# Kernel tuning notes

Hardware: AMD Instinct MI355X
Metric: run time of the kernel (lower is better)

Reference implementation:

```python
import jax, jax.numpy as jnp
import numpy as np

N = 100000      # nodes
E = 1600000     # edges (before self-loops)
IN = 128        # in_size
H = 4           # heads
C = 32          # out_size // heads
OUT = H * C     # 128
NEG_SLOPE = 0.2
LN_EPS = 1e-5
SM_EPS = 1e-16  # PyG softmax eps


def setup_inputs() -> dict:
    key = jax.random.key(0)
    ks = jax.random.split(key, 6)
    x = jax.random.normal(ks[0], (N, IN), dtype=jnp.float32)
    edge_index = jax.random.randint(ks[1], (2, E), 0, N, dtype=jnp.int64)
    W = jax.random.normal(ks[2], (IN, OUT), dtype=jnp.float32) * 0.05
    a_src = jax.random.normal(ks[3], (H, C), dtype=jnp.float32) * 0.05
    a_dst = jax.random.normal(ks[4], (H, C), dtype=jnp.float32) * 0.05
    bias = jnp.zeros((OUT,), dtype=jnp.float32)
    gamma = jnp.ones((OUT,), dtype=jnp.float32)
    beta = jnp.zeros((OUT,), dtype=jnp.float32)
    return {"x": x, "edge_index": edge_index, "W": W, "a_src": a_src,
            "a_dst": a_dst, "bias": bias, "gamma": gamma, "beta": beta}


def reference(x, edge_index, W, a_src, a_dst, bias, gamma, beta):
    n = x.shape[0]
    # add self loops (PyG GATConv default)
    loops = jnp.arange(n, dtype=edge_index.dtype)
    src = jnp.concatenate([edge_index[0], loops])  # [E+N]
    dst = jnp.concatenate([edge_index[1], loops])

    h = (x @ W).reshape(n, H, C)                   # [N,H,C]
    alpha_src = jnp.sum(h * a_src, axis=-1)        # [N,H]
    alpha_dst = jnp.sum(h * a_dst, axis=-1)        # [N,H]

    e = jax.nn.leaky_relu(alpha_src[src] + alpha_dst[dst], NEG_SLOPE)  # [E+N,H]
    # segment softmax over edges grouped by destination node
    emax = jax.ops.segment_max(e, dst, num_segments=n)
    emax = jnp.where(jnp.isfinite(emax), emax, 0.0)
    ee = jnp.exp(e - emax[dst])
    denom = jax.ops.segment_sum(ee, dst, num_segments=n)
    alpha = ee / (denom[dst] + SM_EPS)             # [E+N,H]

    msg = h[src] * alpha[:, :, None]               # [E+N,H,C]
    out = jax.ops.segment_sum(msg, dst, num_segments=n).reshape(n, OUT) + bias

    # LayerNorm(out_size)
    mu = jnp.mean(out, axis=-1, keepdims=True)
    var = jnp.var(out, axis=-1, keepdims=True)
    out = (out - mu) * jax.lax.rsqrt(var + LN_EPS) * gamma + beta
    return jax.nn.relu(out)
```

## Files before the change

kernel.cpp:

```cpp
#include <hip/hip_runtime.h>
#include <hip/hip_bf16.h>
#include <math.h>

#define IN_DIM 128
#define OUT_DIM 128
#define NHEAD 4
#define HC 32
#define NEG_SLOPE 0.2f
#define LN_EPS 1e-5f
#define SM_EPS 1e-16f

#define NB_SHIFT 9
#define BDST 512
#define NBUCK_MAX 256
#define BIN_ITER 28
#define BIN_CHUNK (BIN_ITER * 256)
#define SRC_BITS 17
#define SRC_MASK ((1u << SRC_BITS) - 1u)
#define BCAP_SHIFT 14
#define BCAP (1 << BCAP_SHIFT)

typedef __attribute__((ext_vector_type(8))) short bf16x8;
typedef __attribute__((ext_vector_type(4))) short short4v;
typedef __attribute__((ext_vector_type(4))) float f32x4;

__device__ __forceinline__ float leaky(float v) { return v > 0.f ? v : NEG_SLOPE * v; }

__device__ __forceinline__ short f2b(float f) {
    __hip_bfloat16 b = __float2bfloat16(f);
    return *reinterpret_cast<short*>(&b);
}
__device__ __forceinline__ float b2f(short s) {
    return __uint_as_float(((unsigned)(unsigned short)s) << 16);
}

__device__ __forceinline__ int swz(int row, int byteInRow) {
    return row * 256 + (byteInRow ^ ((row & 7) << 4));
}

__global__ void k_prepW(const float* __restrict__ W, __hip_bfloat16* __restrict__ WtB,
                        int* __restrict__ bcur)
{
    int t0 = blockIdx.x * 256 + threadIdx.x;
    int k = t0 >> 7, j = t0 & 127;
    WtB[j * IN_DIM + k] = __float2bfloat16(W[t0]);
    if (blockIdx.x == 0) bcur[threadIdx.x] = 0;
}

__global__ void __launch_bounds__(256)
k_gemm_bin(const float* __restrict__ x, const __hip_bfloat16* __restrict__ WtB,
           const float* __restrict__ a_src, const float* __restrict__ a_dst,
           __hip_bfloat16* __restrict__ hB, float* __restrict__ asrc_out,
           float* __restrict__ adst_out,
           const int* __restrict__ ei, int* __restrict__ bcur,
           unsigned* __restrict__ binned,
           int E, int N, int nblk_bin)
{
    __shared__ __align__(16) char lds[49152];
    const int t = threadIdx.x;

    if ((int)blockIdx.x < nblk_bin) {
        int* cnt = (int*)lds;
        int* gb  = (int*)(lds + 1024);
        int tot = E + N;
        int base = (int)blockIdx.x * BIN_CHUNK;

        cnt[t] = 0;
        __syncthreads();

        int rk[BIN_ITER], bk[BIN_ITER], dlo[BIN_ITER];
        #pragma unroll
        for (int k = 0; k < BIN_ITER; ++k) {
            int e = base + k * 256 + t;
            bk[k] = -1; rk[k] = 0; dlo[k] = 0;
            if (e < tot) {
                int d = (e < E) ? ei[E + e] : (e - E);
                bk[k] = d >> NB_SHIFT;
                dlo[k] = d & (BDST - 1);
                rk[k] = atomicAdd(&cnt[bk[k]], 1);
            }
        }
        __syncthreads();
        gb[t] = cnt[t] ? ((t << BCAP_SHIFT) + atomicAdd(&bcur[t], cnt[t])) : 0;
        __syncthreads();
        #pragma unroll
        for (int k = 0; k < BIN_ITER; ++k) {
            int e = base + k * 256 + t;
            if (e < tot) {
                int s = (e < E) ? ei[e] : (e - E);
                binned[gb[bk[k]] + rk[k]] = (unsigned)s | ((unsigned)dlo[k] << SRC_BITS);
            }
        }
    } else {
        const int node0 = ((int)blockIdx.x - nblk_bin) * 64;

        #pragma unroll
        for (int i = 0; i < 16; ++i) {
            int idx = (i * 256 + t) * 4;
            int col = idx >> 7, k = idx & 127;
            short4v w4 = *reinterpret_cast<const short4v*>((const short*)WtB + idx);
            *reinterpret_cast<short4v*>(lds + 16384 + swz(col, 2 * k)) = w4;
        }
        #pragma unroll
        for (int i = 0; i < 8; ++i) {
            int idx = (i * 256 + t) * 4;
            int row = idx >> 7, k = idx & 127;
            int node = node0 + row;
            float4 xv = make_float4(0.f, 0.f, 0.f, 0.f);
            if (node < N) xv = *reinterpret_cast<const float4*>(x + (size_t)node * IN_DIM + k);
            short4v xb = { f2b(xv.x), f2b(xv.y), f2b(xv.z), f2b(xv.w) };
            *reinterpret_cast<short4v*>(lds + swz(row, 2 * k)) = xb;
        }
        __syncthreads();

        const int wave = t >> 6, l = t & 63;
        const int lr = l & 15, lg = l >> 4;

        bf16x8 afrag[4];
        #pragma unroll
        for (int kk = 0; kk < 4; ++kk)
            afrag[kk] = *reinterpret_cast<bf16x8*>(lds + swz(wave * 16 + lr, kk * 64 + lg * 16));

        f32x4 acc[8];
        #pragma unroll
        for (int cg = 0; cg < 8; ++cg) acc[cg] = (f32x4){0.f, 0.f, 0.f, 0.f};

        #pragma unroll
        for (int cg = 0; cg < 8; ++cg) {
            #pragma unroll
            for (int kk = 0; kk < 4; ++kk) {
                bf16x8 b = *reinterpret_cast<bf16x8*>(lds + 16384 + swz(cg * 16 + lr, kk * 64 + lg * 16));
                acc[cg] = __builtin_amdgcn_mfma_f32_16x16x32_bf16(afrag[kk], b, acc[cg], 0, 0, 0);
            }
        }

        __syncthreads();
        #pragma unroll
        for (int q = 0; q < 4; ++q) {
            int row = wave * 16 + lg * 4 + q;
            #pragma unroll
            for (int cg = 0; cg < 8; ++cg)
                *reinterpret_cast<short*>(lds + swz(row, (cg * 16 + lr) * 2)) = f2b(acc[cg][q]);
        }
        __syncthreads();

        {
            int row = t >> 2;
            int node = node0 + row;
            int head = t & 3;
            if (node < N) {
                char* dst = (char*)(hB + (size_t)node * OUT_DIM);
                const float4* asv = (const float4*)(a_src + head * HC);
                const float4* adv = (const float4*)(a_dst + head * HC);
                float s = 0.f, dd = 0.f;
                #pragma unroll
                for (int c = 0; c < 4; ++c) {
                    int bir = head * 64 + c * 16;
                    bf16x8 vv = *reinterpret_cast<bf16x8*>(lds + swz(row, bir));
                    *reinterpret_cast<bf16x8*>(dst + bir) = vv;
                    float4 a0 = asv[c * 2], a1 = asv[c * 2 + 1];
                    float4 d0 = adv[c * 2], d1 = adv[c * 2 + 1];
                    s  = fmaf(b2f(vv[0]), a0.x, s);  dd = fmaf(b2f(vv[0]), d0.x, dd);
                    s  = fmaf(b2f(vv[1]), a0.y, s);  dd = fmaf(b2f(vv[1]), d0.y, dd);
                    s  = fmaf(b2f(vv[2]), a0.z, s);  dd = fmaf(b2f(vv[2]), d0.z, dd);
                    s  = fmaf(b2f(vv[3]), a0.w, s);  dd = fmaf(b2f(vv[3]), d0.w, dd);
                    s  = fmaf(b2f(vv[4]), a1.x, s);  dd = fmaf(b2f(vv[4]), d1.x, dd);
                    s  = fmaf(b2f(vv[5]), a1.y, s);  dd = fmaf(b2f(vv[5]), d1.y, dd);
                    s  = fmaf(b2f(vv[6]), a1.z, s);  dd = fmaf(b2f(vv[6]), d1.z, dd);
                    s  = fmaf(b2f(vv[7]), a1.w, s);  dd = fmaf(b2f(vv[7]), d1.w, dd);
                }
                asrc_out[node * NHEAD + head] = s;
                adst_out[node * NHEAD + head] = dd;
            }
        }
    }
}

__global__ void k_bucket_csr(const unsigned* __restrict__ binned, const int* __restrict__ bcur,
                             int* __restrict__ rowbeg, int* __restrict__ rowend,
                             int* __restrict__ csr_src, int N)
{
    __shared__ int cnt[BDST];
    __shared__ int s2[256];
    int b = blockIdx.x;
    int t = threadIdx.x;
    int d0 = b << NB_SHIFT;
    int base = b << BCAP_SHIFT;
    int ne = bcur[b];

    cnt[t] = 0; cnt[t + 256] = 0;
    __syncthreads();
    for (int i = t; i < ne; i += 256) {
        unsigned p = binned[base + i];
        atomicAdd(&cnt[p >> SRC_BITS], 1);
    }
    __syncthreads();
    int c0 = cnt[2 * t], c1 = cnt[2 * t + 1];
    s2[t] = c0 + c1;
    __syncthreads();
    #pragma unroll
    for (int off = 1; off < 256; off <<= 1) {
        int tmp = (t >= off) ? s2[t - off] : 0;
        __syncthreads();
        s2[t] += tmp;
        __syncthreads();
    }
    int e0 = (t ? s2[t - 1] : 0);
    cnt[2 * t] = e0;
    cnt[2 * t + 1] = e0 + c0;
    if (d0 + 2 * t < N) {
        rowbeg[d0 + 2 * t] = base + e0;
        rowend[d0 + 2 * t] = base + e0 + c0;
    }
    if (d0 + 2 * t + 1 < N) {
        rowbeg[d0 + 2 * t + 1] = base + e0 + c0;
        rowend[d0 + 2 * t + 1] = base + e0 + c0 + c1;
    }
    __syncthreads();
    for (int i = t; i < ne; i += 256) {
        unsigned p = binned[base + i];
        int r = atomicAdd(&cnt[p >> SRC_BITS], 1);
        csr_src[base + r] = (int)(p & SRC_MASK);
    }
}

__global__ void k_gather(const int* __restrict__ csr_src,
                         const int* __restrict__ rowbeg, const int* __restrict__ rowend,
                         const __hip_bfloat16* __restrict__ hB,
                         const float* __restrict__ asrc, const float* __restrict__ adst,
                         const float* __restrict__ bias, const float* __restrict__ gamma,
                         const float* __restrict__ beta, float* __restrict__ out, int N)
{
    int wave = threadIdx.x >> 6;
    int l = threadIdx.x & 63;
    int d = blockIdx.x * 4 + wave;
    if (d >= N) return;
    int head = l >> 4;
    const char* hp = (const char*)hB;
    unsigned voff = (unsigned)(l << 2);
    float ad = adst[d * NHEAD + head];
    int beg = __builtin_amdgcn_readfirstlane(rowbeg[d]);
    int end = __builtin_amdgcn_readfirstlane(rowend[d]);

    float ax0 = 0.f, ay0 = 0.f, dn0 = 0.f;
    float ax1 = 0.f, ay1 = 0.f, dn1 = 0.f;

    int idx = beg + (l & 15);
    int cl = idx < end ? idx : end - 1;
    int smine = csr_src[cl];
    float v = (idx < end) ? asrc[(unsigned)smine * NHEAD + head] : -1e30f;

    for (int c = beg; c < end; c += 16) {
        float ee = __expf(leaky(v + ad));
        int scur = smine;
        int c2 = c + 16;
        if (c2 < end) {
            int idx2 = c2 + (l & 15);
            int cl2 = idx2 < end ? idx2 : end - 1;
            smine = csr_src[cl2];
            v = (idx2 < end) ? asrc[(unsigned)smine * NHEAD + head] : -1e30f;
        }

#define GLOAD(E_)                                                                     \
        unsigned se##E_ = (unsigned)__builtin_amdgcn_readlane(scur, (E_));            \
        unsigned hv##E_ = *(const unsigned*)(hp + ((se##E_ << 8) + voff));
#define GCONS(E_, AX_, AY_, DN_) {                                                    \
        float eb = __int_as_float(__builtin_amdgcn_ds_swizzle(                        \
            __float_as_int(ee), 0x10 | ((E_) << 5)));                                 \
        AX_ = fmaf(eb, __uint_as_float(hv##E_ << 16), AX_);                           \
        AY_ = fmaf(eb, __uint_as_float(hv##E_ & 0xffff0000u), AY_);  DN_ += eb;       \
    }
        { GLOAD(0) GLOAD(1) GLOAD(2) GLOAD(3) GLOAD(4) GLOAD(5) GLOAD(6) GLOAD(7)
          GCONS(0, ax0, ay0, dn0) GCONS(1, ax1, ay1, dn1)
          GCONS(2, ax0, ay0, dn0) GCONS(3, ax1, ay1, dn1)
          GCONS(4, ax0, ay0, dn0) GCONS(5, ax1, ay1, dn1)
          GCONS(6, ax0, ay0, dn0) GCONS(7, ax1, ay1, dn1) }
        { GLOAD(8) GLOAD(9) GLOAD(10) GLOAD(11) GLOAD(12) GLOAD(13) GLOAD(14) GLOAD(15)
          GCONS(8, ax0, ay0, dn0)  GCONS(9, ax1, ay1, dn1)
          GCONS(10, ax0, ay0, dn0) GCONS(11, ax1, ay1, dn1)
          GCONS(12, ax0, ay0, dn0) GCONS(13, ax1, ay1, dn1)
          GCONS(14, ax0, ay0, dn0) GCONS(15, ax1, ay1, dn1) }
#undef GLOAD
#undef GCONS
    }

    float accx = ax0 + ax1, accy = ay0 + ay1, den = dn0 + dn1;
    float inv = 1.f / (den + SM_EPS);
    float vx = accx * inv + bias[2 * l];
    float vy = accy * inv + bias[2 * l + 1];

    float s1 = vx + vy;
    float s2 = vx * vx + vy * vy;
    #pragma unroll
    for (int m = 32; m >= 1; m >>= 1) {
        s1 += __shfl_xor(s1, m, 64);
        s2 += __shfl_xor(s2, m, 64);
    }
    float mean = s1 * (1.f / OUT_DIM);
    float var = s2 * (1.f / OUT_DIM) - mean * mean;
    float r = rsqrtf(var + LN_EPS);
    float ox = (vx - mean) * r * gamma[2 * l] + beta[2 * l];
    float oy = (vy - mean) * r * gamma[2 * l + 1] + beta[2 * l + 1];
    ox = ox > 0.f ? ox : 0.f;
    oy = oy > 0.f ? oy : 0.f;
    *reinterpret_cast<float2*>(&out[(size_t)d * OUT_DIM + 2 * l]) = make_float2(ox, oy);
}

extern "C" void kernel_launch(void* const* d_in, const int* in_sizes, int n_in,
                              void* d_out, int out_size, void* d_ws, size_t ws_size,
                              hipStream_t stream) {
    const float* x      = (const float*)d_in[0];
    const int*   ei     = (const int*)d_in[1];
    const float* W      = (const float*)d_in[2];
    const float* a_src  = (const float*)d_in[3];
    const float* a_dst  = (const float*)d_in[4];
    const float* bias   = (const float*)d_in[5];
    const float* gamma  = (const float*)d_in[6];
    const float* beta   = (const float*)d_in[7];
    float* out = (float*)d_out;

    const int N = in_sizes[0] / IN_DIM;
    const int E = in_sizes[1] / 2;
    const int TOT = E + N;
    const int nbuck = (N + BDST - 1) >> NB_SHIFT;
    const int nblk_gemm = (N + 63) / 64;
    const int nblk_bin = (TOT + BIN_CHUNK - 1) / BIN_CHUNK;

    char* p = (char*)d_ws;
    __hip_bfloat16* hB = (__hip_bfloat16*)p;  p += (size_t)N * OUT_DIM * sizeof(__hip_bfloat16);
    __hip_bfloat16* WtB = (__hip_bfloat16*)p; p += (size_t)IN_DIM * OUT_DIM * sizeof(__hip_bfloat16);
    float* asrc   = (float*)p;                p += (size_t)N * NHEAD * sizeof(float);
    float* adst   = (float*)p;                p += (size_t)N * NHEAD * sizeof(float);
    int* bcur     = (int*)p;                  p += NBUCK_MAX * sizeof(int);
    int* rowbeg   = (int*)p;                  p += (size_t)N * sizeof(int);
    int* rowend   = (int*)p;                  p += (size_t)N * sizeof(int);
    unsigned* binned = (unsigned*)p;          p += (size_t)nbuck * BCAP * sizeof(unsigned);
    int* csr_src  = (int*)p;                  p += (size_t)nbuck * BCAP * sizeof(int);

    k_prepW<<<64, 256, 0, stream>>>(W, WtB, bcur);
    k_gemm_bin<<<nblk_bin + nblk_gemm, 256, 0, stream>>>(x, WtB, a_src, a_dst, hB, asrc, adst,
                                                         ei, bcur, binned, E, N, nblk_bin);
    k_bucket_csr<<<nbuck, 256, 0, stream>>>(binned, bcur, rowbeg, rowend, csr_src, N);
    k_gather<<<(N + 3) / 4, 256, 0, stream>>>(csr_src, rowbeg, rowend, hB, asrc, adst,
                                              bias, gamma, beta, out, N);
}
```

Baseline: 150.8 us.

## Restructure gather so each 16-lane group handles separate edges with 16-byte row loads

The gather kernel now assigns each quarter-wave (16 lanes) its own edge, and each lane loads 8 bf16 features (16 bytes) instead of one 4-byte pair. This replaces readlane/ds_swizzle broadcasts of indices and weights. Each lane also computes its own attention logit and exp directly, and source indices are prefetched as an int4 vector. The four partial accumulators are combined with cross-slot shuffles before the LayerNorm, which uses a 16-lane reduction, and only one slot writes the output. The aim is wider memory transactions and fewer cross-lane operations, at the cost of redundant asrc loads and exps per lane and a possibly unaligned int4 load of csr_src.

New measurement: 158.6 us. 5.2% more time.

```diff
diff --git a/kernel.cpp b/kernel.cpp
--- a/kernel.cpp
+++ b/kernel.cpp
@@ -23,6 +23,7 @@
 typedef __attribute__((ext_vector_type(8))) short bf16x8;
 typedef __attribute__((ext_vector_type(4))) short short4v;
 typedef __attribute__((ext_vector_type(4))) float f32x4;
+typedef int int4u __attribute__((ext_vector_type(4), aligned(4)));
 
 __device__ __forceinline__ float leaky(float v) { return v > 0.f ? v : NEG_SLOPE * v; }
 
@@ -235,75 +236,91 @@
     int l = threadIdx.x & 63;
     int d = blockIdx.x * 4 + wave;
     if (d >= N) return;
-    int head = l >> 4;
+    int csl = l & 15;
+    int eslot = l >> 4;
+    int head = csl >> 2;
     const char* hp = (const char*)hB;
-    unsigned voff = (unsigned)(l << 2);
+    unsigned hvoff = (unsigned)(csl << 4);
     float ad = adst[d * NHEAD + head];
     int beg = __builtin_amdgcn_readfirstlane(rowbeg[d]);
     int end = __builtin_amdgcn_readfirstlane(rowend[d]);
-
-    float ax0 = 0.f, ay0 = 0.f, dn0 = 0.f;
-    float ax1 = 0.f, ay1 = 0.f, dn1 = 0.f;
-
-    int idx = beg + (l & 15);
-    int cl = idx < end ? idx : end - 1;
-    int smine = csr_src[cl];
-    float v = (idx < end) ? asrc[(unsigned)smine * NHEAD + head] : -1e30f;
+    unsigned sfix = (unsigned)csr_src[beg];
+
+    float a0 = 0.f, a1 = 0.f, a2 = 0.f, a3 = 0.f;
+    float a4 = 0.f, a5 = 0.f, a6 = 0.f, a7 = 0.f;
+    float den = 0.f;
+
+    int4u s4 = *reinterpret_cast<const int4u*>(csr_src + beg + eslot * 4);
 
     for (int c = beg; c < end; c += 16) {
-        float ee = __expf(leaky(v + ad));
-        int scur = smine;
-        int c2 = c + 16;
-        if (c2 < end) {
-            int idx2 = c2 + (l & 15);
-            int cl2 = idx2 < end ? idx2 : end - 1;
-            smine = csr_src[cl2];
-            v = (idx2 < end) ? asrc[(unsigned)smine * NHEAD + head] : -1e30f;
-        }
-
-#define GLOAD(E_)                                                                     \
-        unsigned se##E_ = (unsigned)__builtin_amdgcn_readlane(scur, (E_));            \
-        unsigned hv##E_ = *(const unsigned*)(hp + ((se##E_ << 8) + voff));
-#define GCONS(E_, AX_, AY_, DN_) {                                                    \
-        float eb = __int_as_float(__builtin_amdgcn_ds_swizzle(                        \
-            __float_as_int(ee), 0x10 | ((E_) << 5)));                                 \
-        AX_ = fmaf(eb, __uint_as_float(hv##E_ << 16), AX_);                           \
-        AY_ = fmaf(eb, __uint_as_float(hv##E_ & 0xffff0000u), AY_);  DN_ += eb;       \
-    }
-        { GLOAD(0) GLOAD(1) GLOAD(2) GLOAD(3) GLOAD(4) GLOAD(5) GLOAD(6) GLOAD(7)
-          GCONS(0, ax0, ay0, dn0) GCONS(1, ax1, ay1, dn1)
-          GCONS(2, ax0, ay0, dn0) GCONS(3, ax1, ay1, dn1)
-          GCONS(4, ax0, ay0, dn0) GCONS(5, ax1, ay1, dn1)
-          GCONS(6, ax0, ay0, dn0) GCONS(7, ax1, ay1, dn1) }
-        { GLOAD(8) GLOAD(9) GLOAD(10) GLOAD(11) GLOAD(12) GLOAD(13) GLOAD(14) GLOAD(15)
-          GCONS(8, ax0, ay0, dn0)  GCONS(9, ax1, ay1, dn1)
-          GCONS(10, ax0, ay0, dn0) GCONS(11, ax1, ay1, dn1)
-          GCONS(12, ax0, ay0, dn0) GCONS(13, ax1, ay1, dn1)
-          GCONS(14, ax0, ay0, dn0) GCONS(15, ax1, ay1, dn1) }
-#undef GLOAD
-#undef GCONS
-    }
-
-    float accx = ax0 + ax1, accy = ay0 + ay1, den = dn0 + dn1;
+        int4u scur = s4;
+        if (c + 16 < end)
+            s4 = *reinterpret_cast<const int4u*>(csr_src + c + 16 + eslot * 4);
+
+#define SUB(S_) {                                                                     \
+        int idxs = c + eslot * 4 + (S_);                                              \
+        unsigned se = (idxs < end) ? (unsigned)scur[S_] : sfix;                       \
+        float va = asrc[se * NHEAD + head];                                           \
+        float ee = (idxs < end) ? __expf(leaky(va + ad)) : 0.f;                       \
+        bf16x8 hq = *reinterpret_cast<const bf16x8*>(hp + ((size_t)se << 8) + hvoff); \
+        a0 = fmaf(ee, b2f(hq[0]), a0);  a1 = fmaf(ee, b2f(hq[1]), a1);                \
+        a2 = fmaf(ee, b2f(hq[2]), a2);  a3 = fmaf(ee, b2f(hq[3]), a3);                \
+        a4 = fmaf(ee, b2f(hq[4]), a4);  a5 = fmaf(ee, b2f(hq[5]), a5);                \
+        a6 = fmaf(ee, b2f(hq[6]), a6);  a7 = fmaf(ee, b2f(hq[7]), a7);                \
+        den += ee;                                                                    \
+    }
+        SUB(0) SUB(1) SUB(2) SUB(3)
+#undef SUB
+    }
+
+    a0 += __shfl_xor(a0, 16, 64);  a0 += __shfl_xor(a0, 32, 64);
+    a1 += __shfl_xor(a1, 16, 64);  a1 += __shfl_xor(a1, 32, 64);
+    a2 += __shfl_xor(a2, 16, 64);  a2 += __shfl_xor(a2, 32, 64);
+    a3 += __shfl_xor(a3, 16, 64);  a3 += __shfl_xor(a3, 32, 64);
+    a4 += __shfl_xor(a4, 16, 64);  a4 += __shfl_xor(a4, 32, 64);
+    a5 += __shfl_xor(a5, 16, 64);  a5 += __shfl_xor(a5, 32, 64);
+    a6 += __shfl_xor(a6, 16, 64);  a6 += __shfl_xor(a6, 32, 64);
+    a7 += __shfl_xor(a7, 16, 64);  a7 += __shfl_xor(a7, 32, 64);
+    den += __shfl_xor(den, 16, 64); den += __shfl_xor(den, 32, 64);
+
     float inv = 1.f / (den + SM_EPS);
-    float vx = accx * inv + bias[2 * l];
-    float vy = accy * inv + bias[2 * l + 1];
-
-    float s1 = vx + vy;
-    float s2 = vx * vx + vy * vy;
+    float4 b0 = *reinterpret_cast<const float4*>(bias + csl * 8);
+    float4 b1 = *reinterpret_cast<const float4*>(bias + csl * 8 + 4);
+    float v0 = a0 * inv + b0.x, v1 = a1 * inv + b0.y;
+    float v2 = a2 * inv + b0.z, v3 = a3 * inv + b0.w;
+    float v4 = a4 * inv + b1.x, v5 = a5 * inv + b1.y;
+    float v6 = a6 * inv + b1.z, v7 = a7 * inv + b1.w;
+
+    float s1 = ((v0 + v1) + (v2 + v3)) + ((v4 + v5) + (v6 + v7));
+    float s2 = ((v0 * v0 + v1 * v1) + (v2 * v2 + v3 * v3)) +
+               ((v4 * v4 + v5 * v5) + (v6 * v6 + v7 * v7));
     #pragma unroll
-    for (int m = 32; m >= 1; m >>= 1) {
+    for (int m = 1; m < 16; m <<= 1) {
         s1 += __shfl_xor(s1, m, 64);
         s2 += __shfl_xor(s2, m, 64);
     }
     float mean = s1 * (1.f / OUT_DIM);
     float var = s2 * (1.f / OUT_DIM) - mean * mean;
     float r = rsqrtf(var + LN_EPS);
-    float ox = (vx - mean) * r * gamma[2 * l] + beta[2 * l];
-    float oy = (vy - mean) * r * gamma[2 * l + 1] + beta[2 * l + 1];
-    ox = ox > 0.f ? ox : 0.f;
-    oy = oy > 0.f ? oy : 0.f;
-    *reinterpret_cast<float2*>(&out[(size_t)d * OUT_DIM + 2 * l]) = make_float2(ox, oy);
+
+    if (eslot == 0) {
+        float4 g0 = *reinterpret_cast<const float4*>(gamma + csl * 8);
+        float4 g1 = *reinterpret_cast<const float4*>(gamma + csl * 8 + 4);
+        float4 e0 = *reinterpret_cast<const float4*>(beta + csl * 8);
+        float4 e1 = *reinterpret_cast<const float4*>(beta + csl * 8 + 4);
+        float4 o0, o1;
+        o0.x = fmaxf((v0 - mean) * r * g0.x + e0.x, 0.f);
+        o0.y = fmaxf((v1 - mean) * r * g0.y + e0.y, 0.f);
+        o0.z = fmaxf((v2 - mean) * r * g0.z + e0.z, 0.f);
+        o0.w = fmaxf((v3 - mean) * r * g0.w + e0.w, 0.f);
+        o1.x = fmaxf((v4 - mean) * r * g1.x + e1.x, 0.f);
+        o1.y = fmaxf((v5 - mean) * r * g1.y + e1.y, 0.f);
+        o1.z = fmaxf((v6 - mean) * r * g1.z + e1.z, 0.f);
+        o1.w = fmaxf((v7 - mean) * r * g1.w + e1.w, 0.f);
+        float* op = out + (size_t)d * OUT_DIM + csl * 8;
+        *reinterpret_cast<float4*>(op) = o0;
+        *reinterpret_cast<float4*>(op + 4) = o1;
+    }
 }
 
 extern "C" void kernel_launch(void* const* d_in, const int* in_sizes, int n_in,
```
